# Optimization experiments

Measured on AMD Instinct MI355X. Metric: run time of the kernel, lower is better.

The kernel has to match this reference:

```python
import jax, jax.numpy as jnp
import numpy as np

DUSER, DACTION, BS = 512, 512, 65536
M = DUSER + DACTION
NUM_STEPS = 200  # original runs range(200) with `if step:` guard -> 199 Adam updates
LR, B1, B2, EPS = 0.1, 0.9, 0.999, 1e-8  # torch.optim.Adam defaults except lr=0.1


def setup_inputs() -> dict:
    key = jax.random.key(0)
    k1, k2, k3 = jax.random.split(key, 3)
    return {
        "mean": jax.random.normal(k1, (M,), dtype=jnp.float32),
        "va": jax.random.normal(k2, (M, M), dtype=jnp.float32),
        "xt": jax.random.normal(k3, (BS, M), dtype=jnp.float32),
    }


def _adam_loop(m_col, va):
    """199 Adam steps on w minimizing f(w)=0.5*(w-m)^T Q (w-m) (+ const).

    Note: in the original, the log-sigmoid term uses `mean` (not w), so it is
    constant w.r.t. w and contributes zero gradient to the Adam updates.
    """
    def loss_w(w):  # f as a function of w (w-dependent part only)
        aa = w - m_col  # (M,1)
        return 0.5 * (aa.T @ va @ aa)[0, 0]

    g_fn = jax.grad(loss_w)
    w0 = jnp.ones((va.shape[0], 1), dtype=jnp.float32)

    def step(carry, t):
        w, mo, vo = carry
        g = g_fn(w)
        mo = B1 * mo + (1.0 - B1) * g
        vo = B2 * vo + (1.0 - B2) * g * g
        mhat = mo / (1.0 - B1 ** t)
        vhat = vo / (1.0 - B2 ** t)
        w = w - LR * mhat / (jnp.sqrt(vhat) + EPS)
        return (w, mo, vo), None

    ts = jnp.arange(1, NUM_STEPS, dtype=jnp.float32)  # bias-correction step counts 1..199
    (w, _, _), _ = jax.lax.scan(step, (w0, jnp.zeros_like(w0), jnp.zeros_like(w0)), ts)
    return w


def reference(mean, va, xt):
    m_col = mean[:, None]  # (M,1)
    w = _adam_loop(m_col, va)  # final w after 199 Adam updates
    aa = w - m_col
    inter1 = -0.5 * (aa.T @ va @ aa)[0, 0]
    # vectorized form of the per-sample loop: sum_i log sigmoid(x_i @ mean)
    inter2 = jnp.sum(jax.nn.log_sigmoid(xt @ m_col))
    return -(inter1 + inter2)  # final value of f at loop exit
```

## Files before the change

### kernel.cpp

```cpp
#include <hip/hip_runtime.h>
#include <math.h>

#define MD 1024
#define NWG_ADAM 16
#define RPB 64
#define RPW 8
#define PW 128
#define BLK 512
#define TOTAL_BLOCKS 256
#define B_BLOCKS (TOTAL_BLOCKS - NWG_ADAM)
#define WAVES_PER_BLOCK (BLK / 64)
#define B_WAVES (B_BLOCKS * WAVES_PER_BLOCK)
#define BS_ROWS 65536
#define POLL_BAIL (1 << 17)

#define WS_I1_F 4096
#define WS_LS_F 4112

typedef unsigned long long u64t;
typedef unsigned int u32x4 __attribute__((ext_vector_type(4)));

__device__ __forceinline__ void tag_store(u64t* p, unsigned gen, float v) {
  u64t x = ((u64t)gen << 32) | (u64t)__float_as_uint(v);
  __hip_atomic_store(p, x, __ATOMIC_RELAXED, __HIP_MEMORY_SCOPE_AGENT);
  asm volatile("" ::: "memory");
}

__device__ __forceinline__ u32x4 poll16(const u64t* p) {
  u32x4 r;
  asm volatile("global_load_dwordx4 %0, %1, off sc0 sc1\n\t"
               "s_waitcnt vmcnt(0)"
               : "=v"(r) : "v"(p) : "memory");
  return r;
}

__device__ __forceinline__ float comb2(float a, float b, int sel, int m) {
  float keep = sel ? b : a;
  float send = sel ? a : b;
  return keep + __shfl_xor(send, m);
}

__device__ __forceinline__ float reduce8(const float p[8], int lane) {
  float c01 = comb2(p[0], p[1], lane & 1, 1);
  float c23 = comb2(p[2], p[3], lane & 1, 1);
  float c45 = comb2(p[4], p[5], lane & 1, 1);
  float c67 = comb2(p[6], p[7], lane & 1, 1);
  float d03 = comb2(c01, c23, lane & 2, 2);
  float d47 = comb2(c45, c67, lane & 2, 2);
  float e   = comb2(d03, d47, lane & 4, 4);
  e += __shfl_xor(e, 8);
  e += __shfl_xor(e, 16);
  e += __shfl_xor(e, 32);
  return e;
}

__global__ __launch_bounds__(BLK, 2) void fused_kernel(
    const float* __restrict__ mean, const float* __restrict__ va,
    const float* __restrict__ xt, float* __restrict__ ws) {
  __shared__ float aas[MD];
  __shared__ float lds8[WAVES_PER_BLOCK];
  const int b = blockIdx.x;
  const int tid = (int)threadIdx.x;
  const int wv = tid >> 6;
  const int lane = tid & 63;

  if (b < NWG_ADAM) {
    u64t* tb = (u64t*)ws;
    const int rbase = b * RPB + wv * RPW;
    float q[8][16];
#pragma unroll
    for (int r = 0; r < 8; ++r)
#pragma unroll
      for (int j = 0; j < 16; ++j)
        q[r][j] = va[(size_t)(rbase + r) * MD + lane + 64 * j];
#pragma unroll
    for (int j = 0; j < 16; ++j) {
      const float* cp = va + (size_t)(lane + 64 * j) * MD + rbase;
      float4 c0 = *(const float4*)cp;
      float4 c1 = *(const float4*)(cp + 4);
      q[0][j] = 0.5f * (q[0][j] + c0.x);
      q[1][j] = 0.5f * (q[1][j] + c0.y);
      q[2][j] = 0.5f * (q[2][j] + c0.z);
      q[3][j] = 0.5f * (q[3][j] + c0.w);
      q[4][j] = 0.5f * (q[4][j] + c1.x);
      q[5][j] = 0.5f * (q[5][j] + c1.y);
      q[6][j] = 0.5f * (q[6][j] + c1.z);
      q[7][j] = 0.5f * (q[7][j] + c1.w);
    }

    const bool owner = (lane < RPW);
    const int myrow = rbase + lane;
    const float mmy = owner ? mean[myrow] : 0.f;
    float wcur = 1.f, mo = 0.f, vo = 0.f;

    if (owner) tag_store(tb + MD + myrow, 1u, 1.f - mmy);

    float pb1 = 1.f, pb2 = 1.f;
    float a[16], p[8];

    for (unsigned t = 1; t <= 200; ++t) {
      pb1 *= 0.9f; pb2 *= 0.999f;
      const float inv1 = 1.f / (1.f - pb1);
      const float inv2 = 1.f / (1.f - pb2);

      {
        const u64t* src = tb + (size_t)(t & 1u) * MD + PW * wv + 2 * lane;
        u32x4 r;
        bool ok;
        int spins = 0;
        do {
          r = poll16(src);
          ok = (r.y == t) & (r.w == t);
          if (++spins > POLL_BAIL) break;
        } while (__any(!ok));
        *(float2*)(aas + PW * wv + 2 * lane) =
            make_float2(__uint_as_float(r.x), __uint_as_float(r.z));
      }
      __syncthreads();
#pragma unroll
      for (int j = 0; j < 16; ++j) a[j] = aas[lane + 64 * j];

#pragma unroll
      for (int r = 0; r < 8; ++r) {
        float s = 0.f;
#pragma unroll
        for (int j = 0; j < 16; ++j) s = fmaf(q[r][j], a[j], s);
        p[r] = s;
      }
      float e = reduce8(p, lane);

      if (t == 200) {
        float contrib = owner ? (wcur - mmy) * e : 0.f;
#pragma unroll
        for (int m = 1; m < 64; m <<= 1) contrib += __shfl_xor(contrib, m);
        if (lane == 0) lds8[wv] = contrib;
        __syncthreads();
        if (tid == 0) {
          float s = 0.f;
#pragma unroll
          for (int i = 0; i < WAVES_PER_BLOCK; ++i) s += lds8[i];
          ws[WS_I1_F + b] = s;
        }
        break;
      }

      if (owner) {
        mo = 0.9f * mo + 0.1f * e;
        vo = 0.999f * vo + 0.001f * (e * e);
        float mhat = mo * inv1;
        float vhat = vo * inv2;
        wcur -= 0.1f * mhat / (sqrtf(vhat) + 1e-8f);
        tag_store(tb + (size_t)((t + 1) & 1u) * MD + myrow, t + 1, wcur - mmy);
      }
    }
  } else {
    const int gw = (b - NWG_ADAM) * WAVES_PER_BLOCK + wv;
    const float4* mp = (const float4*)mean;
    float4 m0 = mp[0 * 64 + lane];
    float4 m1 = mp[1 * 64 + lane];
    float4 m2 = mp[2 * 64 + lane];
    float4 m3 = mp[3 * 64 + lane];
    float lsum = 0.f;
    for (int row = gw; row < BS_ROWS; row += B_WAVES) {
      const float4* xr = (const float4*)(xt + (size_t)row * MD);
      float4 x0 = xr[0 * 64 + lane];
      float4 x1 = xr[1 * 64 + lane];
      float4 x2 = xr[2 * 64 + lane];
      float4 x3 = xr[3 * 64 + lane];
      float acc = 0.f;
      acc = fmaf(x0.x, m0.x, acc); acc = fmaf(x0.y, m0.y, acc);
      acc = fmaf(x0.z, m0.z, acc); acc = fmaf(x0.w, m0.w, acc);
      acc = fmaf(x1.x, m1.x, acc); acc = fmaf(x1.y, m1.y, acc);
      acc = fmaf(x1.z, m1.z, acc); acc = fmaf(x1.w, m1.w, acc);
      acc = fmaf(x2.x, m2.x, acc); acc = fmaf(x2.y, m2.y, acc);
      acc = fmaf(x2.z, m2.z, acc); acc = fmaf(x2.w, m2.w, acc);
      acc = fmaf(x3.x, m3.x, acc); acc = fmaf(x3.y, m3.y, acc);
      acc = fmaf(x3.z, m3.z, acc); acc = fmaf(x3.w, m3.w, acc);
#pragma unroll
      for (int m = 1; m < 64; m <<= 1) acc += __shfl_xor(acc, m);
      if (lane == 0) {
        float z = fminf(acc, 0.f);
        lsum += z - log1pf(expf(-fabsf(acc)));
      }
    }
    if (lane == 0) lds8[wv] = lsum;
    __syncthreads();
    if (tid == 0) {
      float s = 0.f;
#pragma unroll
      for (int i = 0; i < WAVES_PER_BLOCK; ++i) s += lds8[i];
      ws[WS_LS_F + (b - NWG_ADAM)] = s;
    }
  }
}

__global__ void finalize_kernel(const float* __restrict__ ws, float* __restrict__ out) {
  const int lane = (int)threadIdx.x & 63;
  float qsum = (lane < NWG_ADAM) ? ws[WS_I1_F + lane] : 0.f;
  float lssum = 0.f;
  for (int i = lane; i < B_BLOCKS; i += 64) lssum += ws[WS_LS_F + i];
#pragma unroll
  for (int m = 1; m < 64; m <<= 1) {
    qsum += __shfl_xor(qsum, m);
    lssum += __shfl_xor(lssum, m);
  }
  if (lane == 0) out[0] = 0.5f * qsum - lssum;
}

extern "C" void kernel_launch(void* const* d_in, const int* in_sizes, int n_in,
                              void* d_out, int out_size, void* d_ws, size_t ws_size,
                              hipStream_t stream) {
  (void)in_sizes; (void)n_in; (void)out_size; (void)ws_size;
  const float* mean = (const float*)d_in[0];
  const float* va   = (const float*)d_in[1];
  const float* xt   = (const float*)d_in[2];
  float* out = (float*)d_out;
  float* ws  = (float*)d_ws;

  (void)hipMemsetAsync(d_ws, 0, 2 * MD * sizeof(u64t), stream);
  fused_kernel<<<TOTAL_BLOCKS, BLK, 0, stream>>>(mean, va, xt, ws);
  finalize_kernel<<<1, 64, 0, stream>>>(ws, out);
}
```

Measured before the change: 451.4 us.

## Co-locate Adam workgroups on one XCC and poll via local L2 first

Each block now picks its role dynamically. The first block's XCC id is elected through an atomic CAS, and the first 16 blocks that land on that XCC become the Adam workers, while every other block handles the log-sigmoid reduction. Tag stores are written both with a plain workgroup-scope store and with an sc0 sc1 store. Pollers first spin a few times on an L2-coherent load (sc0 only), which only sees the other workers' writes if they share that XCC's L2, and then fall back to the system-coherent poll. The aim is to cut the latency of the cross-workgroup handoff in each of the 200 serial Adam steps. The risks are that fewer than 16 blocks may land on the chosen XCC, leaving Adam rows unassigned and the kernel hanging until the poll bail-out, and that every block now pays for extra atomics at startup.

```diff
diff --git a/kernel.cpp b/kernel.cpp
--- a/kernel.cpp
+++ b/kernel.cpp
@@ -13,25 +13,42 @@
 #define B_WAVES (B_BLOCKS * WAVES_PER_BLOCK)
 #define BS_ROWS 65536
 #define POLL_BAIL (1 << 17)
-
-#define WS_I1_F 4096
-#define WS_LS_F 4112
+#define FAST_SPINS 8
+
+#define WS_EL_F 4096
+#define WS_I1_F 4112
+#define WS_LS_F 4128
 
 typedef unsigned long long u64t;
 typedef unsigned int u32x4 __attribute__((ext_vector_type(4)));
 
 __device__ __forceinline__ void tag_store(u64t* p, unsigned gen, float v) {
   u64t x = ((u64t)gen << 32) | (u64t)__float_as_uint(v);
-  __hip_atomic_store(p, x, __ATOMIC_RELAXED, __HIP_MEMORY_SCOPE_AGENT);
+  __hip_atomic_store(p, x, __ATOMIC_RELAXED, __HIP_MEMORY_SCOPE_WORKGROUP);
+  asm volatile("global_store_dwordx2 %0, %1, off sc0 sc1"
+               :: "v"(p), "v"(x) : "memory");
   asm volatile("" ::: "memory");
 }
 
-__device__ __forceinline__ u32x4 poll16(const u64t* p) {
+__device__ __forceinline__ u32x4 poll16_l2(const u64t* p) {
+  u32x4 r;
+  asm volatile("global_load_dwordx4 %0, %1, off sc0\n\t"
+               "s_waitcnt vmcnt(0)"
+               : "=v"(r) : "v"(p) : "memory");
+  return r;
+}
+__device__ __forceinline__ u32x4 poll16_llc(const u64t* p) {
   u32x4 r;
   asm volatile("global_load_dwordx4 %0, %1, off sc0 sc1\n\t"
                "s_waitcnt vmcnt(0)"
                : "=v"(r) : "v"(p) : "memory");
   return r;
+}
+
+__device__ __forceinline__ unsigned read_xcc_id() {
+  unsigned x;
+  asm volatile("s_getreg_b32 %0, hwreg(HW_REG_XCC_ID)" : "=s"(x));
+  return x & 7u;
 }
 
 __device__ __forceinline__ float comb2(float a, float b, int sel, int m) {
@@ -59,12 +76,31 @@
     const float* __restrict__ xt, float* __restrict__ ws) {
   __shared__ float aas[MD];
   __shared__ float lds8[WAVES_PER_BLOCK];
-  const int b = blockIdx.x;
+  __shared__ unsigned role_s, idx_s;
   const int tid = (int)threadIdx.x;
   const int wv = tid >> 6;
   const int lane = tid & 63;
 
-  if (b < NWG_ADAM) {
+  if (tid == 0) {
+    unsigned* el = (unsigned*)(ws + WS_EL_F);
+    unsigned xcc = read_xcc_id();
+    unsigned prev = atomicCAS(&el[0], 0u, xcc + 1u);
+    unsigned chosen = (prev == 0u) ? xcc : (prev - 1u);
+    unsigned role = 1, idx;
+    if (xcc == chosen) {
+      unsigned t = atomicAdd(&el[1], 1u);
+      if (t < NWG_ADAM) { role = 0; idx = t; }
+      else idx = atomicAdd(&el[2], 1u);
+    } else {
+      idx = atomicAdd(&el[2], 1u);
+    }
+    role_s = role; idx_s = idx;
+  }
+  __syncthreads();
+  const unsigned role = role_s;
+  const int b = (int)idx_s;
+
+  if (role == 0) {
     u64t* tb = (u64t*)ws;
     const int rbase = b * RPB + wv * RPW;
     float q[8][16];
@@ -107,12 +143,19 @@
         const u64t* src = tb + (size_t)(t & 1u) * MD + PW * wv + 2 * lane;
         u32x4 r;
         bool ok;
-        int spins = 0;
+        int s1 = 0;
         do {
-          r = poll16(src);
+          r = poll16_l2(src);
           ok = (r.y == t) & (r.w == t);
-          if (++spins > POLL_BAIL) break;
-        } while (__any(!ok));
+        } while (!__all(ok) && ++s1 < FAST_SPINS);
+        if (!__all(ok)) {
+          int spins = 0;
+          do {
+            r = poll16_llc(src);
+            ok = (r.y == t) & (r.w == t);
+            if (++spins > POLL_BAIL) break;
+          } while (__any(!ok));
+        }
         *(float2*)(aas + PW * wv + 2 * lane) =
             make_float2(__uint_as_float(r.x), __uint_as_float(r.z));
       }
@@ -154,7 +197,7 @@
       }
     }
   } else {
-    const int gw = (b - NWG_ADAM) * WAVES_PER_BLOCK + wv;
+    const int gw = b * WAVES_PER_BLOCK + wv;
     const float4* mp = (const float4*)mean;
     float4 m0 = mp[0 * 64 + lane];
     float4 m1 = mp[1 * 64 + lane];
@@ -189,7 +232,7 @@
       float s = 0.f;
 #pragma unroll
       for (int i = 0; i < WAVES_PER_BLOCK; ++i) s += lds8[i];
-      ws[WS_LS_F + (b - NWG_ADAM)] = s;
+      ws[WS_LS_F + b] = s;
     }
   }
 }
@@ -217,7 +260,7 @@
   float* out = (float*)d_out;
   float* ws  = (float*)d_ws;
 
-  (void)hipMemsetAsync(d_ws, 0, 2 * MD * sizeof(u64t), stream);
+  (void)hipMemsetAsync(d_ws, 0, (WS_I1_F) * sizeof(float), stream);
   fused_kernel<<<TOTAL_BLOCKS, BLK, 0, stream>>>(mean, va, xt, ws);
   finalize_kernel<<<1, 64, 0, stream>>>(ws, out);
 }
```

New measurement: 823.4 us. +82.4%, slower.
